# Kernel optimization log

Measured on AMD Instinct MI355X. Metric: run time of the kernel, lower is better.

The kernel has to match this reference:

```python
import jax, jax.numpy as jnp
import numpy as np

HEADS = 48
HEAD_DIM = 64
DIM = 3072
RANK = 128
TEXT_LEN = 226
VID_LEN = 1822
B = 1
LORA_W = 1.0
EPS = 1e-5


def setup_inputs() -> dict:
    key = jax.random.key(0)
    ks = jax.random.split(key, 24)
    s = 0.02  # weight init scale
    inp = {
        "hidden_states": jax.random.normal(ks[0], (B, VID_LEN, DIM), jnp.float32),
        "encoder_hidden_states": jax.random.normal(ks[1], (B, TEXT_LEN, DIM), jnp.float32),
        "rope_cos": jax.random.uniform(ks[2], (VID_LEN, HEAD_DIM), jnp.float32),
        "rope_sin": jax.random.uniform(ks[3], (VID_LEN, HEAD_DIM), jnp.float32),
        "Wq": jax.random.normal(ks[4], (DIM, DIM), jnp.float32) * s,
        "bq": jax.random.normal(ks[5], (DIM,), jnp.float32) * s,
        "Wk": jax.random.normal(ks[6], (DIM, DIM), jnp.float32) * s,
        "bk": jax.random.normal(ks[7], (DIM,), jnp.float32) * s,
        "Wv": jax.random.normal(ks[8], (DIM, DIM), jnp.float32) * s,
        "bv": jax.random.normal(ks[9], (DIM,), jnp.float32) * s,
        "Wo": jax.random.normal(ks[10], (DIM, DIM), jnp.float32) * s,
        "bo": jax.random.normal(ks[11], (DIM,), jnp.float32) * s,
        "lq_down": jax.random.normal(ks[12], (RANK, DIM), jnp.float32) / RANK,
        "lq_up": jax.random.normal(ks[13], (DIM, RANK), jnp.float32) * s,
        "lk_down": jax.random.normal(ks[14], (RANK, DIM), jnp.float32) / RANK,
        "lk_up": jax.random.normal(ks[15], (DIM, RANK), jnp.float32) * s,
        "lv_down": jax.random.normal(ks[16], (RANK, DIM), jnp.float32) / RANK,
        "lv_up": jax.random.normal(ks[17], (DIM, RANK), jnp.float32) * s,
        "lp_down": jax.random.normal(ks[18], (RANK, DIM), jnp.float32) / RANK,
        "lp_up": jax.random.normal(ks[19], (DIM, RANK), jnp.float32) * s,
        "gamma_q": jnp.ones((HEAD_DIM,), jnp.float32),
        "beta_q": jnp.zeros((HEAD_DIM,), jnp.float32),
        "gamma_k": jnp.ones((HEAD_DIM,), jnp.float32),
        "beta_k": jnp.zeros((HEAD_DIM,), jnp.float32),
    }
    return inp


def _lora(x, down, up):
    # x: [B,S,DIM]; down: [RANK,DIM]; up: [DIM,RANK]
    return (x @ down.T) @ up.T


def _layernorm(x, gamma, beta):
    mu = jnp.mean(x, axis=-1, keepdims=True)
    var = jnp.mean(jnp.square(x - mu), axis=-1, keepdims=True)
    return (x - mu) * jax.lax.rsqrt(var + EPS) * gamma + beta


def _apply_rope(x, cos, sin):
    # diffusers apply_rotary_emb, use_real=True, unbind_dim=-1
    # x: [B,H,S,D]; cos/sin: [S,D]
    xr = x.reshape(*x.shape[:-1], HEAD_DIM // 2, 2)
    x1, x2 = xr[..., 0], xr[..., 1]
    x_rot = jnp.stack([-x2, x1], axis=-1).reshape(x.shape)
    return x * cos + x_rot * sin


def reference(hidden_states, encoder_hidden_states, rope_cos, rope_sin,
              Wq, bq, Wk, bk, Wv, bv, Wo, bo,
              lq_down, lq_up, lk_down, lk_up, lv_down, lv_up, lp_down, lp_up,
              gamma_q, beta_q, gamma_k, beta_k):
    h = jnp.concatenate([encoder_hidden_states, hidden_states], axis=1)  # [B,S,DIM]
    S = h.shape[1]

    q = h @ Wq.T + bq + _lora(h, lq_down, lq_up) * LORA_W
    k = h @ Wk.T + bk + _lora(h, lk_down, lk_up) * LORA_W
    v = h @ Wv.T + bv + _lora(h, lv_down, lv_up) * LORA_W

    def split_heads(x):  # [B,S,DIM] -> [B,H,S,D]
        return x.reshape(B, S, HEADS, HEAD_DIM).transpose(0, 2, 1, 3)

    q, k, v = split_heads(q), split_heads(k), split_heads(v)
    q = _layernorm(q, gamma_q, beta_q)
    k = _layernorm(k, gamma_k, beta_k)

    # RoPE on video tokens only
    q = q.at[:, :, TEXT_LEN:].set(_apply_rope(q[:, :, TEXT_LEN:], rope_cos, rope_sin))
    k = k.at[:, :, TEXT_LEN:].set(_apply_rope(k[:, :, TEXT_LEN:], rope_cos, rope_sin))

    # scaled dot-product attention (no mask, no dropout)
    scale = 1.0 / np.sqrt(HEAD_DIM).astype(np.float32)
    scores = jnp.einsum("bhqd,bhkd->bhqk", q, k) * scale
    probs = jax.nn.softmax(scores, axis=-1)
    attn_out = jnp.einsum("bhqk,bhkd->bhqd", probs, v)

    out = attn_out.transpose(0, 2, 1, 3).reshape(B, S, DIM)
    out = out @ Wo.T + bo + _lora(out, lp_down, lp_up) * LORA_W

    enc_out = out[:, :TEXT_LEN, :]
    hid_out = out[:, TEXT_LEN:, :]
    return (hid_out, enc_out)
```

## Files before the change

### kernel.cpp

```cpp
#include <hip/hip_runtime.h>
#include <hip/hip_bf16.h>
#include <stdint.h>

#define S_TOT 2048
#define TEXT 226
#define VID 1822
#define DIM 3072
#define NH 48
#define HD 64

typedef __bf16 bf16x8 __attribute__((ext_vector_type(8)));
typedef __bf16 bf16x4 __attribute__((ext_vector_type(4)));
typedef float f32x4 __attribute__((ext_vector_type(4)));

#define AS1 __attribute__((address_space(1)))
#define AS3 __attribute__((address_space(3)))

__device__ __forceinline__ void g2l16(const void* g, void* l) {
    __builtin_amdgcn_global_load_lds((const AS1 uint32_t*)(uintptr_t)g,
                                     (AS3 uint32_t*)(uintptr_t)l, 16, 0, 0);
}

__device__ __forceinline__ f32x4 mfma16(bf16x4 a, bf16x4 b, f32x4 c) {
#if __has_builtin(__builtin_amdgcn_mfma_f32_16x16x16bf16_1k)
    typedef short s4 __attribute__((ext_vector_type(4)));
    union U { bf16x4 b; s4 s; };
    U ua, ub; ua.b = a; ub.b = b;
    return __builtin_amdgcn_mfma_f32_16x16x16bf16_1k(ua.s, ub.s, c, 0, 0, 0);
#else
    f32x4 d = c;
    asm volatile("v_mfma_f32_16x16x16_bf16 %0, %1, %2, %0"
                 : "+v"(d) : "v"(a), "v"(b));
    return d;
#endif
}

#define ARENA_N 47431680ull

struct NormArgs { const void* p[24]; };

__global__ __launch_bounds__(256)
void normalize_inputs(NormArgs a, __bf16* __restrict__ arena)
{
    static constexpr unsigned long long segStart[25] = {
        0ull, 694272ull, 6291456ull, 15728640ull, 25165824ull, 34603008ull,
        44040192ull, 44433408ull, 44826624ull, 45219840ull, 45613056ull,
        46006272ull, 46399488ull, 46792704ull, 47185920ull, 47302528ull,
        47419136ull, 47422208ull, 47425280ull, 47428352ull, 47431424ull,
        47431488ull, 47431552ull, 47431616ull, 47431680ull };
    static constexpr int segIn[24] = {
        1, 0, 4, 6, 8, 10, 12, 13, 14, 15, 16, 17, 18, 19, 2, 3,
        5, 7, 9, 11, 20, 21, 22, 23 };

    const uint32_t w0 = *(const uint32_t*)a.p[20];
    const bool f32in = (w0 == 0x3F800000u);

    const size_t i0 = ((size_t)blockIdx.x * 256 + threadIdx.x) * 8;
    if (i0 >= ARENA_N) return;
    int s = 0;
    while (i0 >= segStart[s + 1]) s++;
    const size_t off = i0 - segStart[s];

    if (f32in) {
        const float* src = (const float*)a.p[segIn[s]] + off;
        const float4 v0 = ((const float4*)src)[0];
        const float4 v1 = ((const float4*)src)[1];
        bf16x8 o;
        o[0] = (__bf16)v0.x; o[1] = (__bf16)v0.y; o[2] = (__bf16)v0.z; o[3] = (__bf16)v0.w;
        o[4] = (__bf16)v1.x; o[5] = (__bf16)v1.y; o[6] = (__bf16)v1.z; o[7] = (__bf16)v1.w;
        *(bf16x8*)(arena + i0) = o;
    } else {
        const __bf16* src = (const __bf16*)a.p[segIn[s]] + off;
        *(uint4*)(arena + i0) = *(const uint4*)src;
    }
}

__device__ __forceinline__ void mm_chunks(
    const __bf16* __restrict__ Ag, int lda, const __bf16* __restrict__ Bg, int ldb,
    int kbeg, int kend, f32x4 (&acc)[4][4], __bf16* As, __bf16* Bs,
    int wave, int srow, int schk, int rdoff, int l15, int wm, int wn)
{
    for (int k0 = kbeg; k0 < kend; k0 += 32) {
        __syncthreads();
#pragma unroll
        for (int i = 0; i < 2; i++) {
            const int blk = i * 4 + wave;
            const int r = blk * 16 + srow;
            g2l16(Ag + (size_t)r * lda + k0 + schk, &As[blk * 512]);
            g2l16(Bg + (size_t)r * ldb + k0 + schk, &Bs[blk * 512]);
        }
        __syncthreads();
        bf16x8 af[4], bfr[4];
#pragma unroll
        for (int i = 0; i < 4; i++)
            af[i] = *(const bf16x8*)&As[(wm + i * 16 + l15) * 32 + rdoff];
#pragma unroll
        for (int j = 0; j < 4; j++)
            bfr[j] = *(const bf16x8*)&Bs[(wn + j * 16 + l15) * 32 + rdoff];
#pragma unroll
        for (int i = 0; i < 4; i++)
#pragma unroll
            for (int j = 0; j < 4; j++)
                acc[i][j] = __builtin_amdgcn_mfma_f32_16x16x32_bf16(af[i], bfr[j], acc[i][j], 0, 0, 0);
    }
}

#define PLANE_ELEMS (2048 * 512)

template<int MODE, bool FUSE2>
__global__ __launch_bounds__(256)
void gemm_bt(const __bf16* __restrict__ A, int lda,
             const __bf16* __restrict__ B0, const __bf16* __restrict__ B1,
             const __bf16* __restrict__ B2, int ldb,
             const __bf16* __restrict__ bias0, const __bf16* __restrict__ bias1,
             const __bf16* __restrict__ bias2,
             const __bf16* __restrict__ A2, int lda2, int a2ColOff,
             const __bf16* __restrict__ U0, const __bf16* __restrict__ U1,
             const __bf16* __restrict__ U2, int ldu,
             float* __restrict__ C, __bf16* __restrict__ Cb, int ldc,
             int K, int K2, int tilesPerGroup, int kChunk,
             void* __restrict__ dout, const void* __restrict__ probe)
{
    __shared__ __bf16 As[128 * 32];
    __shared__ __bf16 Bs[128 * 32];
    const int tid  = threadIdx.x;
    const int wave = tid >> 6;
    const int lane = tid & 63;
    const int l15  = lane & 15, quad = lane >> 4;
    const int bm = blockIdx.x, bn = blockIdx.y;
    const int group = bn / tilesPerGroup;
    const int nt    = bn - group * tilesPerGroup;
    const __bf16* B    = (group == 0) ? B0 : ((group == 1) ? B1 : B2);
    const __bf16* bias = (group == 0) ? bias0 : ((group == 1) ? bias1 : bias2);

    const int k0s = blockIdx.z * kChunk;
    int k0e = k0s + kChunk; if (k0e > K) k0e = K;

    const int srow  = lane >> 2;
    const int schk  = ((((lane & 3) - (lane >> 3)) & 3)) * 8;
    const int rdoff = ((quad + (l15 >> 1)) & 3) * 8;
    const __bf16* Ag = A + (size_t)(bm * 128) * lda;
    const __bf16* Bg = B + (size_t)(nt * 128) * ldb;

    f32x4 acc[4][4] = {};
    const int wm = (wave & 1) * 64;
    const int wn = (wave >> 1) * 64;

    mm_chunks(Ag, lda, Bg, ldb, k0s, k0e, acc, As, Bs, wave, srow, schk, rdoff, l15, wm, wn);

    if (FUSE2) {
        const __bf16* U = (group == 0) ? U0 : ((group == 1) ? U1 : U2);
        const __bf16* A2g = A2 + group * a2ColOff + (size_t)(bm * 128) * lda2;
        const __bf16* Ug  = U + (size_t)(nt * 128) * ldu;
        mm_chunks(A2g, lda2, Ug, ldu, 0, K2, acc, As, Bs, wave, srow, schk, rdoff, l15, wm, wn);
    }

    bool f32out = false;
    if (MODE == 1) f32out = (*(const uint32_t*)probe == 0x3F800000u);
    float* Cz = (MODE == 0) ? (C + (size_t)blockIdx.z * PLANE_ELEMS) : C;

#pragma unroll
    for (int i = 0; i < 4; i++) {
#pragma unroll
        for (int j = 0; j < 4; j++) {
            const int coll = wn + j * 16 + l15;
            const int col  = bn * 128 + coll;
            float bv = 0.f;
            if (bias) bv = (float)bias[nt * 128 + coll];
#pragma unroll
            for (int r = 0; r < 4; r++) {
                const int row = bm * 128 + wm + i * 16 + quad * 4 + r;
                float v = acc[i][j][r] + bv;
                if (MODE == 1) {
                    const size_t mrow = (row < TEXT) ? (size_t)(row + VID) : (size_t)(row - TEXT);
                    if (f32out) ((float*)dout)[mrow * DIM + col] = v;
                    else        ((__bf16*)dout)[mrow * DIM + col] = (__bf16)v;
                } else if (MODE == 3) {
                    Cb[(size_t)row * ldc + col] = (__bf16)v;
                } else {
                    Cz[(size_t)row * ldc + col] = v;
                }
            }
        }
    }
}

__global__ __launch_bounds__(256)
void ln_rope(const __bf16* __restrict__ qkv,
             const __bf16* __restrict__ gq, const __bf16* __restrict__ bq,
             const __bf16* __restrict__ gk, const __bf16* __restrict__ bk,
             const __bf16* __restrict__ cosb, const __bf16* __restrict__ sinb,
             __bf16* __restrict__ qh, __bf16* __restrict__ kh)
{
    const int s = blockIdx.x;
    const int wave = threadIdx.x >> 6, lane = threadIdx.x & 63;
    for (int idx = wave; idx < 2 * NH; idx += 4) {
        const int mat  = idx / NH;
        const int head = idx - mat * NH;
        float x = (float)qkv[(size_t)s * 9216 + mat * DIM + head * HD + lane];
        float mu = x;
        mu += __shfl_xor(mu, 1, 64);  mu += __shfl_xor(mu, 2, 64);
        mu += __shfl_xor(mu, 4, 64);  mu += __shfl_xor(mu, 8, 64);
        mu += __shfl_xor(mu, 16, 64); mu += __shfl_xor(mu, 32, 64);
        mu *= 0.015625f;
        float d = x - mu;
        float vv = d * d;
        vv += __shfl_xor(vv, 1, 64);  vv += __shfl_xor(vv, 2, 64);
        vv += __shfl_xor(vv, 4, 64);  vv += __shfl_xor(vv, 8, 64);
        vv += __shfl_xor(vv, 16, 64); vv += __shfl_xor(vv, 32, 64);
        vv *= 0.015625f;
        const float g = (float)(mat ? gk[lane] : gq[lane]);
        const float b = (float)(mat ? bk[lane] : bq[lane]);
        float y = d * rsqrtf(vv + 1e-5f) * g + b;
        if (s >= TEXT) {
            const int pos = s - TEXT;
            const float c  = (float)cosb[pos * HD + lane];
            const float sn = (float)sinb[pos * HD + lane];
            const float oth = __shfl_xor(y, 1, 64);
            const float rot = (lane & 1) ? oth : -oth;
            y = y * c + rot * sn;
        }
        if (mat == 0) y *= 0.125f;
        __bf16* dst = mat ? kh : qh;
        dst[((size_t)head * S_TOT + s) * HD + lane] = (__bf16)y;
    }
}

__global__ __launch_bounds__(256)
void vtrans(const __bf16* __restrict__ qkv, __bf16* __restrict__ vt)
{
    __shared__ float tile[64][65];
    const int h = blockIdx.x, sb = blockIdx.y;
    const int tid = threadIdx.x;
    const int r0 = tid >> 4;
    const int c0 = (tid & 15) * 4;
#pragma unroll
    for (int p = 0; p < 4; p++) {
        const int r = p * 16 + r0;
        const uint2 raw = *(const uint2*)&qkv[((size_t)(sb * 64 + r)) * 9216 + 2 * DIM + h * HD + c0];
        const __bf16* b = (const __bf16*)&raw;
#pragma unroll
        for (int e = 0; e < 4; e++) tile[r][c0 + e] = (float)b[e];
    }
    __syncthreads();
#pragma unroll
    for (int p = 0; p < 4; p++) {
        const int d = p * 16 + r0;
        __bf16 o[4];
#pragma unroll
        for (int e = 0; e < 4; e++) o[e] = (__bf16)tile[c0 + e][d];
        *(uint2*)&vt[((size_t)(h * HD + d)) * S_TOT + sb * 64 + c0] = *(const uint2*)o;
    }
}

#define KS_LD 72
#define VS_LD 136
#define NKB (S_TOT / 128)

__device__ __forceinline__ void fa_load(const __bf16* __restrict__ kh,
                                        const __bf16* __restrict__ vt,
                                        int h, int kb, int tid,
                                        bf16x8 (&kr)[4], bf16x8 (&vr)[4])
{
#pragma unroll
    for (int p = 0; p < 4; p++) {
        const int id = p * 256 + tid;
        const int krow = id >> 3, kc = (id & 7) * 8;
        kr[p] = *(const bf16x8*)(kh + ((size_t)(h * S_TOT + kb * 128 + krow)) * HD + kc);
        const int vrow = id >> 4, vc = (id & 15) * 8;
        vr[p] = *(const bf16x8*)(vt + ((size_t)(h * HD + vrow)) * S_TOT + kb * 128 + vc);
    }
}

__global__ __launch_bounds__(256)
void flash_attn(const __bf16* __restrict__ qh, const __bf16* __restrict__ kh,
                const __bf16* __restrict__ vt, __bf16* __restrict__ outp)
{
    __shared__ __bf16 Ks[128 * KS_LD];
    __shared__ __bf16 Vs[64 * VS_LD];
    const int qb = blockIdx.x, h = blockIdx.y;
    const int tid = threadIdx.x, wave = tid >> 6, lane = tid & 63;
    const int l15 = lane & 15, quad = lane >> 4;

    const __bf16* qp = qh + ((size_t)(h * S_TOT + qb * 64 + wave * 16 + l15)) * HD + quad * 8;
    const bf16x8 qf0 = *(const bf16x8*)qp;
    const bf16x8 qf1 = *(const bf16x8*)(qp + 32);

    f32x4 of[4] = {};
    float m_i = -1e30f, l_i = 0.f;
    const float L2E = 1.44269504f;

    bf16x8 kr[4], vr[4];
    fa_load(kh, vt, h, 0, tid, kr, vr);

    for (int kb = 0; kb < NKB; kb++) {
        __syncthreads();
#pragma unroll
        for (int p = 0; p < 4; p++) {
            const int id = p * 256 + tid;
            const int krow = id >> 3, kc = (id & 7) * 8;
            *(bf16x8*)&Ks[krow * KS_LD + kc] = kr[p];
            const int vrow = id >> 4, vc = (id & 15) * 8;
            *(bf16x8*)&Vs[vrow * VS_LD + vc] = vr[p];
        }
        __syncthreads();
        if (kb + 1 < NKB) fa_load(kh, vt, h, kb + 1, tid, kr, vr);

        f32x4 sf[8];
#pragma unroll
        for (int n = 0; n < 8; n++) {
            const bf16x8 k0 = *(const bf16x8*)&Ks[(n * 16 + l15) * KS_LD + quad * 8];
            const bf16x8 k1 = *(const bf16x8*)&Ks[(n * 16 + l15) * KS_LD + 32 + quad * 8];
            f32x4 z = {0.f, 0.f, 0.f, 0.f};
            z = __builtin_amdgcn_mfma_f32_16x16x32_bf16(k0, qf0, z, 0, 0, 0);
            sf[n] = __builtin_amdgcn_mfma_f32_16x16x32_bf16(k1, qf1, z, 0, 0, 0);
        }

        float mx = sf[0][0];
#pragma unroll
        for (int n = 0; n < 8; n++)
#pragma unroll
            for (int r = 0; r < 4; r++) mx = fmaxf(mx, sf[n][r]);
        mx = fmaxf(mx, __shfl_xor(mx, 16, 64));
        mx = fmaxf(mx, __shfl_xor(mx, 32, 64));
        const float mnew = fmaxf(m_i, mx);
        const float alpha = __builtin_amdgcn_exp2f((m_i - mnew) * L2E);
        m_i = mnew;
        float rs = 0.f;
#pragma unroll
        for (int n = 0; n < 8; n++)
#pragma unroll
            for (int r = 0; r < 4; r++) {
                const float pv = __builtin_amdgcn_exp2f((sf[n][r] - mnew) * L2E);
                sf[n][r] = pv;
                rs += pv;
            }
        rs += __shfl_xor(rs, 16, 64);
        rs += __shfl_xor(rs, 32, 64);
        l_i = l_i * alpha + rs;

        bf16x4 pf[8];
#pragma unroll
        for (int kk = 0; kk < 8; kk++) {
            bf16x4 o;
            o[0] = (__bf16)sf[kk][0]; o[1] = (__bf16)sf[kk][1];
            o[2] = (__bf16)sf[kk][2]; o[3] = (__bf16)sf[kk][3];
            pf[kk] = o;
        }

#pragma unroll
        for (int r = 0; r < 4; r++) {
            const float a_r = __shfl(alpha, quad * 4 + r, 16);
#pragma unroll
            for (int j = 0; j < 4; j++) of[j][r] *= a_r;
        }

#pragma unroll
        for (int kk = 0; kk < 8; kk++) {
#pragma unroll
            for (int j = 0; j < 4; j++) {
                const bf16x4 vf = *(const bf16x4*)&Vs[(j * 16 + l15) * VS_LD + kk * 16 + quad * 4];
                of[j] = mfma16(pf[kk], vf, of[j]);
            }
        }
    }

#pragma unroll
    for (int r = 0; r < 4; r++) {
        const float lr = __shfl(l_i, quad * 4 + r, 16);
        const float inv = 1.f / lr;
        const int row = qb * 64 + wave * 16 + quad * 4 + r;
#pragma unroll
        for (int j = 0; j < 4; j++)
            outp[(size_t)row * DIM + h * HD + j * 16 + l15] = (__bf16)(of[j][r] * inv);
    }
}

__global__ __launch_bounds__(256)
void reduce4_bf16(const float* __restrict__ src, __bf16* __restrict__ dst, int n4)
{
    const int i = blockIdx.x * blockDim.x + threadIdx.x;
    if (i < n4) {
        const float4 a = ((const float4*)src)[i];
        const float4 b = ((const float4*)(src + PLANE_ELEMS))[i];
        const float4 c = ((const float4*)(src + 2 * PLANE_ELEMS))[i];
        const float4 d = ((const float4*)(src + 3 * PLANE_ELEMS))[i];
        __bf16 o[4] = {(__bf16)(a.x + b.x + c.x + d.x), (__bf16)(a.y + b.y + c.y + d.y),
                       (__bf16)(a.z + b.z + c.z + d.z), (__bf16)(a.w + b.w + c.w + d.w)};
        ((uint2*)dst)[i] = *(const uint2*)o;
    }
}

extern "C" void kernel_launch(void* const* d_in, const int* in_sizes, int n_in,
                              void* d_out, int out_size, void* d_ws, size_t ws_size,
                              hipStream_t stream)
{
    char* ws = (char*)d_ws;
    __bf16* arena = (__bf16*)ws;

    const __bf16* h     = arena + 0;
    const __bf16* Wq    = arena + 6291456;
    const __bf16* Wk    = arena + 15728640;
    const __bf16* Wv    = arena + 25165824;
    const __bf16* Wo    = arena + 34603008;
    const __bf16* lqd   = arena + 44040192;
    const __bf16* lqu   = arena + 44433408;
    const __bf16* lkd   = arena + 44826624;
    const __bf16* lku   = arena + 45219840;
    const __bf16* lvd   = arena + 45613056;
    const __bf16* lvu   = arena + 46006272;
    const __bf16* lpd   = arena + 46399488;
    const __bf16* lpu   = arena + 46792704;
    const __bf16* ropec = arena + 47185920;
    const __bf16* ropes = arena + 47302528;
    const __bf16* bq    = arena + 47419136;
    const __bf16* bk    = arena + 47422208;
    const __bf16* bv    = arena + 47425280;
    const __bf16* bo    = arena + 47428352;
    const __bf16* gq    = arena + 47431424;
    const __bf16* btq   = arena + 47431488;
    const __bf16* gk    = arena + 47431552;
    const __bf16* btk   = arena + 47431616;

    __bf16* qkvb = (__bf16*)(ws + 94863360);
    float*  t32  = (float*)(ws + 132612096);
    __bf16* t16  = (__bf16*)(ws + 149389312);
    __bf16* qh   = (__bf16*)(ws + 151486464);
    __bf16* kh   = (__bf16*)(ws + 164069376);
    __bf16* vt   = (__bf16*)(ws + 176652288);
    __bf16* attn = (__bf16*)(ws + 0);

    NormArgs na;
    for (int i = 0; i < 24; i++) na.p[i] = d_in[i];
    normalize_inputs<<<(unsigned)((ARENA_N / 8 + 255) / 256), 256, 0, stream>>>(na, arena);

    gemm_bt<0, false><<<dim3(16, 3, 4), 256, 0, stream>>>(
        h, DIM, lqd, lkd, lvd, DIM, nullptr, nullptr, nullptr,
        nullptr, 0, 0, nullptr, nullptr, nullptr, 0,
        t32, nullptr, 512, DIM, 0, 1, 768, nullptr, nullptr);
    reduce4_bf16<<<(2048 * 512 / 4 + 255) / 256, 256, 0, stream>>>(t32, t16, 2048 * 512 / 4);

    gemm_bt<3, true><<<dim3(16, 72, 1), 256, 0, stream>>>(
        h, DIM, Wq, Wk, Wv, DIM, bq, bk, bv,
        t16, 512, 128, lqu, lku, lvu, 128,
        nullptr, qkvb, 9216, DIM, 128, 24, DIM, nullptr, nullptr);

    ln_rope<<<2048, 256, 0, stream>>>(qkvb, gq, btq, gk, btk, ropec, ropes, qh, kh);
    vtrans<<<dim3(48, 32), 256, 0, stream>>>(qkvb, vt);
    flash_attn<<<dim3(32, 48), 256, 0, stream>>>(qh, kh, vt, attn);

    gemm_bt<0, false><<<dim3(16, 1, 4), 256, 0, stream>>>(
        attn, DIM, lpd, lpd, lpd, DIM, nullptr, nullptr, nullptr,
        nullptr, 0, 0, nullptr, nullptr, nullptr, 0,
        t32 + 384, nullptr, 512, DIM, 0, 1, 768, nullptr, nullptr);
    reduce4_bf16<<<(2048 * 512 / 4 + 255) / 256, 256, 0, stream>>>(t32, t16, 2048 * 512 / 4);

    gemm_bt<1, true><<<dim3(16, 24, 1), 256, 0, stream>>>(
        attn, DIM, Wo, Wo, Wo, DIM, bo, bo, bo,
        t16 + 384, 512, 0, lpu, lpu, lpu, 128,
        nullptr, nullptr, DIM, DIM, 128, 24, DIM, d_out, d_in[20]);
}
```

Before: 716.7 us.

## Fold LoRA adapters into dense weights and merge LN/RoPE with V transpose

Each call now precomputes W' = W + up·down for the Q, K, V and O projections. It transposes the LoRA down matrices and runs a small K=128 GEMM that adds the result onto the base weight. This removes the split-K LoRA down-projection GEMMs, the fp32 reduce kernels and the extra K=128 pass inside the main projection GEMMs. The LN/RoPE kernel and the V transpose are merged into one launch. The trade is extra full-size weight read and write traffic for the fold, and the folded sum is rounded to bf16 before use.

```diff
diff --git a/kernel.cpp b/kernel.cpp
--- a/kernel.cpp
+++ b/kernel.cpp
@@ -105,20 +105,14 @@
     }
 }
 
-#define PLANE_ELEMS (2048 * 512)
-
-template<int MODE, bool FUSE2>
+template<int MODE>
 __global__ __launch_bounds__(256)
 void gemm_bt(const __bf16* __restrict__ A, int lda,
              const __bf16* __restrict__ B0, const __bf16* __restrict__ B1,
              const __bf16* __restrict__ B2, int ldb,
              const __bf16* __restrict__ bias0, const __bf16* __restrict__ bias1,
              const __bf16* __restrict__ bias2,
-             const __bf16* __restrict__ A2, int lda2, int a2ColOff,
-             const __bf16* __restrict__ U0, const __bf16* __restrict__ U1,
-             const __bf16* __restrict__ U2, int ldu,
-             float* __restrict__ C, __bf16* __restrict__ Cb, int ldc,
-             int K, int K2, int tilesPerGroup, int kChunk,
+             __bf16* __restrict__ Cb, int ldc, int K, int tilesPerGroup,
              void* __restrict__ dout, const void* __restrict__ probe)
 {
     __shared__ __bf16 As[128 * 32];
@@ -133,9 +127,6 @@
     const __bf16* B    = (group == 0) ? B0 : ((group == 1) ? B1 : B2);
     const __bf16* bias = (group == 0) ? bias0 : ((group == 1) ? bias1 : bias2);
 
-    const int k0s = blockIdx.z * kChunk;
-    int k0e = k0s + kChunk; if (k0e > K) k0e = K;
-
     const int srow  = lane >> 2;
     const int schk  = ((((lane & 3) - (lane >> 3)) & 3)) * 8;
     const int rdoff = ((quad + (l15 >> 1)) & 3) * 8;
@@ -146,18 +137,10 @@
     const int wm = (wave & 1) * 64;
     const int wn = (wave >> 1) * 64;
 
-    mm_chunks(Ag, lda, Bg, ldb, k0s, k0e, acc, As, Bs, wave, srow, schk, rdoff, l15, wm, wn);
-
-    if (FUSE2) {
-        const __bf16* U = (group == 0) ? U0 : ((group == 1) ? U1 : U2);
-        const __bf16* A2g = A2 + group * a2ColOff + (size_t)(bm * 128) * lda2;
-        const __bf16* Ug  = U + (size_t)(nt * 128) * ldu;
-        mm_chunks(A2g, lda2, Ug, ldu, 0, K2, acc, As, Bs, wave, srow, schk, rdoff, l15, wm, wn);
-    }
+    mm_chunks(Ag, lda, Bg, ldb, 0, K, acc, As, Bs, wave, srow, schk, rdoff, l15, wm, wn);
 
     bool f32out = false;
     if (MODE == 1) f32out = (*(const uint32_t*)probe == 0x3F800000u);
-    float* Cz = (MODE == 0) ? (C + (size_t)blockIdx.z * PLANE_ELEMS) : C;
 
 #pragma unroll
     for (int i = 0; i < 4; i++) {
@@ -175,81 +158,154 @@
                     const size_t mrow = (row < TEXT) ? (size_t)(row + VID) : (size_t)(row - TEXT);
                     if (f32out) ((float*)dout)[mrow * DIM + col] = v;
                     else        ((__bf16*)dout)[mrow * DIM + col] = (__bf16)v;
-                } else if (MODE == 3) {
+                } else {
                     Cb[(size_t)row * ldc + col] = (__bf16)v;
-                } else {
-                    Cz[(size_t)row * ldc + col] = v;
                 }
             }
         }
     }
 }
 
+struct TpArgs { const __bf16* S[4]; __bf16* D[4]; };
+
 __global__ __launch_bounds__(256)
-void ln_rope(const __bf16* __restrict__ qkv,
-             const __bf16* __restrict__ gq, const __bf16* __restrict__ bq,
-             const __bf16* __restrict__ gk, const __bf16* __restrict__ bk,
-             const __bf16* __restrict__ cosb, const __bf16* __restrict__ sinb,
-             __bf16* __restrict__ qh, __bf16* __restrict__ kh)
-{
-    const int s = blockIdx.x;
-    const int wave = threadIdx.x >> 6, lane = threadIdx.x & 63;
-    for (int idx = wave; idx < 2 * NH; idx += 4) {
-        const int mat  = idx / NH;
-        const int head = idx - mat * NH;
-        float x = (float)qkv[(size_t)s * 9216 + mat * DIM + head * HD + lane];
-        float mu = x;
-        mu += __shfl_xor(mu, 1, 64);  mu += __shfl_xor(mu, 2, 64);
-        mu += __shfl_xor(mu, 4, 64);  mu += __shfl_xor(mu, 8, 64);
-        mu += __shfl_xor(mu, 16, 64); mu += __shfl_xor(mu, 32, 64);
-        mu *= 0.015625f;
-        float d = x - mu;
-        float vv = d * d;
-        vv += __shfl_xor(vv, 1, 64);  vv += __shfl_xor(vv, 2, 64);
-        vv += __shfl_xor(vv, 4, 64);  vv += __shfl_xor(vv, 8, 64);
-        vv += __shfl_xor(vv, 16, 64); vv += __shfl_xor(vv, 32, 64);
-        vv *= 0.015625f;
-        const float g = (float)(mat ? gk[lane] : gq[lane]);
-        const float b = (float)(mat ? bk[lane] : bq[lane]);
-        float y = d * rsqrtf(vv + 1e-5f) * g + b;
-        if (s >= TEXT) {
-            const int pos = s - TEXT;
-            const float c  = (float)cosb[pos * HD + lane];
-            const float sn = (float)sinb[pos * HD + lane];
-            const float oth = __shfl_xor(y, 1, 64);
-            const float rot = (lane & 1) ? oth : -oth;
-            y = y * c + rot * sn;
-        }
-        if (mat == 0) y *= 0.125f;
-        __bf16* dst = mat ? kh : qh;
-        dst[((size_t)head * S_TOT + s) * HD + lane] = (__bf16)y;
-    }
-}
+void transp_ld(TpArgs a)
+{
+    __shared__ float tile[64][65];
+    const __bf16* src = a.S[blockIdx.z];
+    __bf16* dst = a.D[blockIdx.z];
+    const int j0 = blockIdx.x * 64;
+    const int r0 = blockIdx.y * 64;
+    const int tid = threadIdx.x;
+    const int rr = tid >> 4;
+    const int cc = (tid & 15) * 4;
+#pragma unroll
+    for (int p = 0; p < 4; p++) {
+        const int r = p * 16 + rr;
+        const uint2 raw = *(const uint2*)&src[(size_t)(r0 + r) * DIM + j0 + cc];
+        const __bf16* b = (const __bf16*)&raw;
+#pragma unroll
+        for (int e = 0; e < 4; e++) tile[r][cc + e] = (float)b[e];
+    }
+    __syncthreads();
+#pragma unroll
+    for (int p = 0; p < 4; p++) {
+        const int j = p * 16 + rr;
+        __bf16 o[4];
+#pragma unroll
+        for (int e = 0; e < 4; e++) o[e] = (__bf16)tile[cc + e][j];
+        *(uint2*)&dst[(size_t)(j0 + j) * 128 + r0 + cc] = *(const uint2*)o;
+    }
+}
+
+struct FoldArgs { const __bf16* A[4]; const __bf16* B[4]; const __bf16* W[4]; __bf16* D[4]; };
 
 __global__ __launch_bounds__(256)
-void vtrans(const __bf16* __restrict__ qkv, __bf16* __restrict__ vt)
+void fold_w(FoldArgs a)
+{
+    __shared__ __bf16 As[128 * 32];
+    __shared__ __bf16 Bs[128 * 32];
+    const int z = blockIdx.z;
+    const int tid  = threadIdx.x;
+    const int wave = tid >> 6;
+    const int lane = tid & 63;
+    const int l15  = lane & 15, quad = lane >> 4;
+    const int bm = blockIdx.x, bn = blockIdx.y;
+
+    const int srow  = lane >> 2;
+    const int schk  = ((((lane & 3) - (lane >> 3)) & 3)) * 8;
+    const int rdoff = ((quad + (l15 >> 1)) & 3) * 8;
+    const __bf16* Ag = a.A[z] + (size_t)(bm * 128) * 128;
+    const __bf16* Bg = a.B[z] + (size_t)(bn * 128) * 128;
+    const __bf16* W  = a.W[z];
+    __bf16* D = a.D[z];
+
+    f32x4 acc[4][4] = {};
+    const int wm = (wave & 1) * 64;
+    const int wn = (wave >> 1) * 64;
+
+    mm_chunks(Ag, 128, Bg, 128, 0, 128, acc, As, Bs, wave, srow, schk, rdoff, l15, wm, wn);
+
+#pragma unroll
+    for (int i = 0; i < 4; i++) {
+#pragma unroll
+        for (int j = 0; j < 4; j++) {
+            const int col = bn * 128 + wn + j * 16 + l15;
+#pragma unroll
+            for (int r = 0; r < 4; r++) {
+                const int row = bm * 128 + wm + i * 16 + quad * 4 + r;
+                const size_t idx = (size_t)row * DIM + col;
+                D[idx] = (__bf16)(acc[i][j][r] + (float)W[idx]);
+            }
+        }
+    }
+}
+
+__global__ __launch_bounds__(256)
+void ln_vt(const __bf16* __restrict__ qkv,
+           const __bf16* __restrict__ gq, const __bf16* __restrict__ bq,
+           const __bf16* __restrict__ gk, const __bf16* __restrict__ bk,
+           const __bf16* __restrict__ cosb, const __bf16* __restrict__ sinb,
+           __bf16* __restrict__ qh, __bf16* __restrict__ kh,
+           __bf16* __restrict__ vt)
 {
     __shared__ float tile[64][65];
-    const int h = blockIdx.x, sb = blockIdx.y;
-    const int tid = threadIdx.x;
-    const int r0 = tid >> 4;
-    const int c0 = (tid & 15) * 4;
-#pragma unroll
-    for (int p = 0; p < 4; p++) {
-        const int r = p * 16 + r0;
-        const uint2 raw = *(const uint2*)&qkv[((size_t)(sb * 64 + r)) * 9216 + 2 * DIM + h * HD + c0];
-        const __bf16* b = (const __bf16*)&raw;
-#pragma unroll
-        for (int e = 0; e < 4; e++) tile[r][c0 + e] = (float)b[e];
-    }
-    __syncthreads();
-#pragma unroll
-    for (int p = 0; p < 4; p++) {
-        const int d = p * 16 + r0;
-        __bf16 o[4];
-#pragma unroll
-        for (int e = 0; e < 4; e++) o[e] = (__bf16)tile[c0 + e][d];
-        *(uint2*)&vt[((size_t)(h * HD + d)) * S_TOT + sb * 64 + c0] = *(const uint2*)o;
+    if (blockIdx.x < 2048) {
+        const int s = blockIdx.x;
+        const int wave = threadIdx.x >> 6, lane = threadIdx.x & 63;
+        for (int idx = wave; idx < 2 * NH; idx += 4) {
+            const int mat  = idx / NH;
+            const int head = idx - mat * NH;
+            float x = (float)qkv[(size_t)s * 9216 + mat * DIM + head * HD + lane];
+            float mu = x;
+            mu += __shfl_xor(mu, 1, 64);  mu += __shfl_xor(mu, 2, 64);
+            mu += __shfl_xor(mu, 4, 64);  mu += __shfl_xor(mu, 8, 64);
+            mu += __shfl_xor(mu, 16, 64); mu += __shfl_xor(mu, 32, 64);
+            mu *= 0.015625f;
+            float d = x - mu;
+            float vv = d * d;
+            vv += __shfl_xor(vv, 1, 64);  vv += __shfl_xor(vv, 2, 64);
+            vv += __shfl_xor(vv, 4, 64);  vv += __shfl_xor(vv, 8, 64);
+            vv += __shfl_xor(vv, 16, 64); vv += __shfl_xor(vv, 32, 64);
+            vv *= 0.015625f;
+            const float g = (float)(mat ? gk[lane] : gq[lane]);
+            const float b = (float)(mat ? bk[lane] : bq[lane]);
+            float y = d * rsqrtf(vv + 1e-5f) * g + b;
+            if (s >= TEXT) {
+                const int pos = s - TEXT;
+                const float c  = (float)cosb[pos * HD + lane];
+                const float sn = (float)sinb[pos * HD + lane];
+                const float oth = __shfl_xor(y, 1, 64);
+                const float rot = (lane & 1) ? oth : -oth;
+                y = y * c + rot * sn;
+            }
+            if (mat == 0) y *= 0.125f;
+            __bf16* dst = mat ? kh : qh;
+            dst[((size_t)head * S_TOT + s) * HD + lane] = (__bf16)y;
+        }
+    } else {
+        const int vb = blockIdx.x - 2048;
+        const int h = vb >> 5, sb = vb & 31;
+        const int tid = threadIdx.x;
+        const int r0 = tid >> 4;
+        const int c0 = (tid & 15) * 4;
+#pragma unroll
+        for (int p = 0; p < 4; p++) {
+            const int r = p * 16 + r0;
+            const uint2 raw = *(const uint2*)&qkv[((size_t)(sb * 64 + r)) * 9216 + 2 * DIM + h * HD + c0];
+            const __bf16* b = (const __bf16*)&raw;
+#pragma unroll
+            for (int e = 0; e < 4; e++) tile[r][c0 + e] = (float)b[e];
+        }
+        __syncthreads();
+#pragma unroll
+        for (int p = 0; p < 4; p++) {
+            const int d = p * 16 + r0;
+            __bf16 o[4];
+#pragma unroll
+            for (int e = 0; e < 4; e++) o[e] = (__bf16)tile[c0 + e][d];
+            *(uint2*)&vt[((size_t)(h * HD + d)) * S_TOT + sb * 64 + c0] = *(const uint2*)o;
+        }
     }
 }
 
@@ -373,21 +429,6 @@
 #pragma unroll
         for (int j = 0; j < 4; j++)
             outp[(size_t)row * DIM + h * HD + j * 16 + l15] = (__bf16)(of[j][r] * inv);
-    }
-}
-
-__global__ __launch_bounds__(256)
-void reduce4_bf16(const float* __restrict__ src, __bf16* __restrict__ dst, int n4)
-{
-    const int i = blockIdx.x * blockDim.x + threadIdx.x;
-    if (i < n4) {
-        const float4 a = ((const float4*)src)[i];
-        const float4 b = ((const float4*)(src + PLANE_ELEMS))[i];
-        const float4 c = ((const float4*)(src + 2 * PLANE_ELEMS))[i];
-        const float4 d = ((const float4*)(src + 3 * PLANE_ELEMS))[i];
-        __bf16 o[4] = {(__bf16)(a.x + b.x + c.x + d.x), (__bf16)(a.y + b.y + c.y + d.y),
-                       (__bf16)(a.z + b.z + c.z + d.z), (__bf16)(a.w + b.w + c.w + d.w)};
-        ((uint2*)dst)[i] = *(const uint2*)o;
     }
 }
 
@@ -422,41 +463,42 @@
     const __bf16* gk    = arena + 47431552;
     const __bf16* btk   = arena + 47431616;
 
-    __bf16* qkvb = (__bf16*)(ws + 94863360);
-    float*  t32  = (float*)(ws + 132612096);
-    __bf16* t16  = (__bf16*)(ws + 149389312);
-    __bf16* qh   = (__bf16*)(ws + 151486464);
-    __bf16* kh   = (__bf16*)(ws + 164069376);
-    __bf16* vt   = (__bf16*)(ws + 176652288);
+    __bf16* ldT  = (__bf16*)(ws + 94863360);
+    __bf16* qkvb = (__bf16*)(ws + 98009088);
+    __bf16* Wpo  = (__bf16*)(ws + 135757824);
+    __bf16* Wpq  = (__bf16*)(ws + 154632192);
+    __bf16* Wpk  = (__bf16*)(ws + 173506560);
+    __bf16* Wpv  = (__bf16*)(ws + 192380928);
+    __bf16* qh   = (__bf16*)(ws + 154632192);
+    __bf16* kh   = (__bf16*)(ws + 179798016);
+    __bf16* vt   = (__bf16*)(ws + 12582912);
     __bf16* attn = (__bf16*)(ws + 0);
 
     NormArgs na;
     for (int i = 0; i < 24; i++) na.p[i] = d_in[i];
     normalize_inputs<<<(unsigned)((ARENA_N / 8 + 255) / 256), 256, 0, stream>>>(na, arena);
 
-    gemm_bt<0, false><<<dim3(16, 3, 4), 256, 0, stream>>>(
-        h, DIM, lqd, lkd, lvd, DIM, nullptr, nullptr, nullptr,
-        nullptr, 0, 0, nullptr, nullptr, nullptr, 0,
-        t32, nullptr, 512, DIM, 0, 1, 768, nullptr, nullptr);
-    reduce4_bf16<<<(2048 * 512 / 4 + 255) / 256, 256, 0, stream>>>(t32, t16, 2048 * 512 / 4);
-
-    gemm_bt<3, true><<<dim3(16, 72, 1), 256, 0, stream>>>(
-        h, DIM, Wq, Wk, Wv, DIM, bq, bk, bv,
-        t16, 512, 128, lqu, lku, lvu, 128,
-        nullptr, qkvb, 9216, DIM, 128, 24, DIM, nullptr, nullptr);
-
-    ln_rope<<<2048, 256, 0, stream>>>(qkvb, gq, btq, gk, btk, ropec, ropes, qh, kh);
-    vtrans<<<dim3(48, 32), 256, 0, stream>>>(qkvb, vt);
+    TpArgs tp;
+    tp.S[0] = lqd; tp.S[1] = lkd; tp.S[2] = lvd; tp.S[3] = lpd;
+    tp.D[0] = ldT; tp.D[1] = ldT + 393216; tp.D[2] = ldT + 786432; tp.D[3] = ldT + 1179648;
+    transp_ld<<<dim3(48, 2, 4), 256, 0, stream>>>(tp);
+
+    FoldArgs fa;
+    fa.A[0] = lqu; fa.A[1] = lku; fa.A[2] = lvu; fa.A[3] = lpu;
+    fa.B[0] = tp.D[0]; fa.B[1] = tp.D[1]; fa.B[2] = tp.D[2]; fa.B[3] = tp.D[3];
+    fa.W[0] = Wq; fa.W[1] = Wk; fa.W[2] = Wv; fa.W[3] = Wo;
+    fa.D[0] = Wpq; fa.D[1] = Wpk; fa.D[2] = Wpv; fa.D[3] = Wpo;
+    fold_w<<<dim3(24, 24, 4), 256, 0, stream>>>(fa);
+
+    gemm_bt<3><<<dim3(16, 72), 256, 0, stream>>>(
+        h, DIM, Wpq, Wpk, Wpv, DIM, bq, bk, bv,
+        qkvb, 9216, DIM, 24, nullptr, nullptr);
+
+    ln_vt<<<2048 + 1536, 256, 0, stream>>>(qkvb, gq, btq, gk, btk, ropec, ropes, qh, kh, vt);
+
     flash_attn<<<dim3(32, 48), 256, 0, stream>>>(qh, kh, vt, attn);
 
-    gemm_bt<0, false><<<dim3(16, 1, 4), 256, 0, stream>>>(
-        attn, DIM, lpd, lpd, lpd, DIM, nullptr, nullptr, nullptr,
-        nullptr, 0, 0, nullptr, nullptr, nullptr, 0,
-        t32 + 384, nullptr, 512, DIM, 0, 1, 768, nullptr, nullptr);
-    reduce4_bf16<<<(2048 * 512 / 4 + 255) / 256, 256, 0, stream>>>(t32, t16, 2048 * 512 / 4);
-
-    gemm_bt<1, true><<<dim3(16, 24, 1), 256, 0, stream>>>(
-        attn, DIM, Wo, Wo, Wo, DIM, bo, bo, bo,
-        t16 + 384, 512, 0, lpu, lpu, lpu, 128,
-        nullptr, nullptr, DIM, DIM, 128, 24, DIM, d_out, d_in[20]);
-}
+    gemm_bt<1><<<dim3(16, 24), 256, 0, stream>>>(
+        attn, DIM, Wpo, Wpo, Wpo, DIM, bo, bo, bo,
+        nullptr, DIM, DIM, 24, d_out, d_in[20]);
+}
```

After: 713.7 us. About the same (-0.4%).
